# Performance work log

Hardware: AMD Instinct MI355X
Metric: run time of the kernel (lower is better)

Reference implementation:

```python
import jax, jax.numpy as jnp
import numpy as np

E = 2048      # embed_size
H = 16        # heads_size
D_HEAD = E // H          # 128
D_ROPE = 32
SPLIT = D_HEAD - D_ROPE  # 96
C = 512       # d_kv_comp
B, S = 2, 2048
ROT_SCALE = 40.0


def _rotary_emb(seq_len):
    # inv_freq has d_rope//4 entries; emb is [S, d_rope//2]
    half = D_ROPE // 2
    inv_freq = 1.0 / (10000.0 ** (jnp.arange(0, half, 2, dtype=jnp.float32) / half))
    t = jnp.arange(seq_len, dtype=jnp.float32) / ROT_SCALE
    freqs = jnp.einsum('i,j->ij', t, inv_freq)
    return jnp.concatenate([freqs, freqs], axis=-1)  # [S, d_rope//2]


def _rotate_half(x):
    x1, x2 = jnp.split(x, 2, axis=-1)
    return jnp.concatenate([-x2, x1], axis=-1)


def _apply_rotary(x, cos, sin):
    rd = cos.shape[-1]
    x_rot, x_base = x[..., :rd], x[..., rd:]
    x_rot = x_rot * cos + _rotate_half(x_rot) * sin
    return jnp.concatenate([x_rot, x_base], axis=-1)


def setup_inputs() -> dict:
    key = jax.random.key(0)
    ks = jax.random.split(key, 10)

    def xav(k, shape):
        fan_in, fan_out = shape
        lim = float(np.sqrt(6.0 / (fan_in + fan_out)))
        return jax.random.uniform(k, shape, jnp.float32, -lim, lim)

    return {
        'h': jax.random.normal(ks[0], (B, S, E), jnp.float32),
        'W_dkv': xav(ks[1], (E, C)), 'b_dkv': jnp.zeros((C,), jnp.float32),
        'W_dq':  xav(ks[2], (E, C)), 'b_dq':  jnp.zeros((C,), jnp.float32),
        'W_uk':  xav(ks[3], (C, H * SPLIT)),  'b_uk': jnp.zeros((H * SPLIT,), jnp.float32),
        'W_uv':  xav(ks[4], (C, H * D_HEAD)), 'b_uv': jnp.zeros((H * D_HEAD,), jnp.float32),
        'W_uq':  xav(ks[5], (C, H * SPLIT)),  'b_uq': jnp.zeros((H * SPLIT,), jnp.float32),
        'W_qr':  xav(ks[6], (C, H * D_ROPE)), 'b_qr': jnp.zeros((H * D_ROPE,), jnp.float32),
        'W_kr':  xav(ks[7], (E, H * D_ROPE)), 'b_kr': jnp.zeros((H * D_ROPE,), jnp.float32),
        'W_out': xav(ks[8], (H * D_HEAD, E)), 'b_out': jnp.zeros((E,), jnp.float32),
    }


def reference(h, W_dkv, b_dkv, W_dq, b_dq, W_uk, b_uk, W_uv, b_uv,
              W_uq, b_uq, W_qr, b_qr, W_kr, b_kr, W_out, b_out):
    Bq, Sq, _ = h.shape
    c_kv = h @ W_dkv + b_dkv                                   # [B,S,C]
    k = (c_kv @ W_uk + b_uk).reshape(Bq, Sq, H, SPLIT)
    v = (c_kv @ W_uv + b_uv).reshape(Bq, Sq, H, D_HEAD)
    c_q = h @ W_dq + b_dq
    q_base = (c_q @ W_uq + b_uq).reshape(Bq, Sq, H, SPLIT)
    q_rot = (c_q @ W_qr + b_qr).reshape(Bq, Sq, H, D_ROPE)

    emb = _rotary_emb(Sq)                                      # [S, d_rope//2]
    cos = jnp.cos(emb)[None, :, None, :]
    sin = jnp.sin(emb)[None, :, None, :]
    q_rot = _apply_rotary(q_rot, cos, sin)
    k_rot = _apply_rotary((h @ W_kr + b_kr).reshape(Bq, Sq, H, D_ROPE), cos, sin)

    q = jnp.concatenate([q_base, q_rot], axis=-1)              # [B,S,H,d_head]
    k_full = jnp.concatenate([k, k_rot], axis=-1)

    scores = jnp.einsum('bqhd,bkhd->bhqk', q, k_full) / jnp.sqrt(jnp.float32(D_HEAD))
    causal = jnp.tril(jnp.ones((Sq, Sq), dtype=bool))
    scores = jnp.where(causal[None, None], scores, -jnp.inf)
    attn = jax.nn.softmax(scores, axis=-1)
    out = jnp.einsum('bhqk,bkhd->bqhd', attn, v).reshape(Bq, Sq, H * D_HEAD)
    out = out @ W_out + b_out
    return out, c_kv, k_rot
```

## Files before the change

kernel.cpp:

```cpp
#include <hip/hip_runtime.h>
#include <hip/hip_bf16.h>

#define B_   2
#define S_   2048
#define E_   2048
#define H_   16
#define DH_  128
#define DR_  32
#define SP_  96
#define C_   512
#define M_   (B_ * S_)

#define LOG2E 1.4426950408889634f

typedef __attribute__((ext_vector_type(8))) short short8;
typedef __attribute__((ext_vector_type(4))) float floatx4;

__device__ __forceinline__ float bfu(unsigned short u) {
  return __uint_as_float((unsigned)u << 16);
}
__device__ __forceinline__ unsigned short f2bf(float f) {
  unsigned u = __float_as_uint(f);
  return (unsigned short)((u + 0x7fff + ((u >> 16) & 1)) >> 16);
}

__device__ __forceinline__ void gload16(const void* g, void* l) {
  __builtin_amdgcn_global_load_lds(
      (const __attribute__((address_space(1))) void*)g,
      (__attribute__((address_space(3))) void*)l, 16, 0, 0);
}

struct TEnt { const float* W; unsigned short* Wt; int K, N, ntiles, nx; };
struct TTab { TEnt e[8]; };

__global__ __launch_bounds__(256) void prep_kernel(
    const float* __restrict__ hsrc, unsigned short* __restrict__ hdst,
    TTab tab) {
  if (blockIdx.x < 8192) {
    size_t i = ((size_t)blockIdx.x * 256 + threadIdx.x) * 4;
    float4 v = *(const float4*)(hsrc + i);
    ushort4 w;
    w.x = f2bf(v.x); w.y = f2bf(v.y); w.z = f2bf(v.z); w.w = f2bf(v.w);
    *(ushort4*)(hdst + i) = w;
    return;
  }
  __shared__ unsigned short T[32][33];
  int rem = blockIdx.x - 8192;
  const float* W = nullptr; unsigned short* Wt = nullptr;
  int K = 0, N = 0, nx = 1;
  bool done = false;
#pragma unroll
  for (int j = 0; j < 8; j++) {
    if (!done) {
      if (rem < tab.e[j].ntiles) {
        W = tab.e[j].W; Wt = tab.e[j].Wt;
        K = tab.e[j].K; N = tab.e[j].N; nx = tab.e[j].nx;
        done = true;
      } else {
        rem -= tab.e[j].ntiles;
      }
    }
  }
  int n0 = (rem % nx) * 32, k0 = (rem / nx) * 32;
  int t = threadIdx.x, lane = t & 31, grp = t >> 5;
#pragma unroll
  for (int p = 0; p < 4; p++) {
    int k = p * 8 + grp;
    T[lane][k] = f2bf(W[(size_t)(k0 + k) * N + n0 + lane]);
  }
  __syncthreads();
#pragma unroll
  for (int p = 0; p < 4; p++) {
    int n = p * 8 + grp;
    Wt[(size_t)(n0 + n) * K + k0 + lane] = T[n][lane];
  }
}

struct Seg {
  float* outF;
  unsigned short* outB;
  const float* bias;
  const float* biasM;
  int orow, chunk, gstride, obase, nstart, ileave;
  float oscale;
};

__device__ __forceinline__ void gemm_body(
    const unsigned short* __restrict__ A, const unsigned short* __restrict__ W,
    int K, int bm, int bn, const Seg& sg) {
  __shared__ unsigned short As0[128 * 32];
  __shared__ unsigned short Bs0[128 * 32];
  __shared__ unsigned short As1[128 * 32];
  __shared__ unsigned short Bs1[128 * 32];
  int tid = threadIdx.x;
  int lane = tid & 63, wave = tid >> 6;
  int l16 = lane & 15, quad = lane >> 4;
  int wm = (wave & 1) * 64, wn = (wave >> 1) * 64;

  floatx4 acc[4][4];
#pragma unroll
  for (int mt = 0; mt < 4; mt++)
#pragma unroll
    for (int nt = 0; nt < 4; nt++) acc[mt][nt] = (floatx4){0.f, 0.f, 0.f, 0.f};

  int c0 = wave * 2, c1 = c0 + 1;
  int srow = lane >> 2, scol = (lane & 3) * 8;
  const unsigned short* Ag0 = A + (size_t)(bm + c0 * 16 + srow) * K + scol;
  const unsigned short* Ag1 = A + (size_t)(bm + c1 * 16 + srow) * K + scol;
  const unsigned short* Bg0 = W + (size_t)(bn + c0 * 16 + srow) * K + scol;
  const unsigned short* Bg1 = W + (size_t)(bn + c1 * 16 + srow) * K + scol;

#define GSTAGE(kk, Asb, Bsb) do {            \
    gload16(Ag0 + (kk), &Asb[c0 * 512]);     \
    gload16(Ag1 + (kk), &Asb[c1 * 512]);     \
    gload16(Bg0 + (kk), &Bsb[c0 * 512]);     \
    gload16(Bg1 + (kk), &Bsb[c1 * 512]); } while (0)

#define GCOMPUTE(Asb, Bsb) do {                                            \
    short8 af[4], bfv[4];                                                  \
    _Pragma("unroll")                                                      \
    for (int mt = 0; mt < 4; mt++)                                         \
      af[mt] = *(const short8*)&Asb[(wm + mt * 16 + l16) * 32 + quad * 8]; \
    _Pragma("unroll")                                                      \
    for (int nt = 0; nt < 4; nt++)                                         \
      bfv[nt] = *(const short8*)&Bsb[(wn + nt * 16 + l16) * 32 + quad * 8];\
    _Pragma("unroll")                                                      \
    for (int mt = 0; mt < 4; mt++)                                         \
      _Pragma("unroll")                                                    \
      for (int nt = 0; nt < 4; nt++)                                       \
        acc[mt][nt] = __builtin_amdgcn_mfma_f32_16x16x32_bf16(             \
            af[mt], bfv[nt], acc[mt][nt], 0, 0, 0); } while (0)

  GSTAGE(0, As0, Bs0);
  __syncthreads();
  for (int k0 = 0; k0 < K; k0 += 64) {
    GSTAGE(k0 + 32, As1, Bs1);
    GCOMPUTE(As0, Bs0);
    __syncthreads();
    if (k0 + 64 < K) GSTAGE(k0 + 64, As0, Bs0);
    GCOMPUTE(As1, Bs1);
    __syncthreads();
  }
#undef GSTAGE
#undef GCOMPUTE

#pragma unroll
  for (int mt = 0; mt < 4; mt++) {
    int m0 = bm + wm + mt * 16 + quad * 4;
    float bm4[4] = {0.f, 0.f, 0.f, 0.f};
    if (sg.biasM) {
#pragma unroll
      for (int r = 0; r < 4; r++) bm4[r] = sg.biasM[m0 + r];
    }
#pragma unroll
    for (int nt = 0; nt < 4; nt++) {
      int n = bn + wn + nt * 16 + l16;
      int nl = n - sg.nstart;
      float bv = sg.biasM ? 0.f : sg.bias[nl];
      int ncol = sg.obase + (nl / sg.chunk) * sg.gstride + (nl % sg.chunk);
      if (sg.ileave)
        ncol = (ncol & ~31) | ((ncol & 15) << 1) | ((ncol >> 4) & 1);
#pragma unroll
      for (int r = 0; r < 4; r++) {
        float val = (acc[mt][nt][r] + (sg.biasM ? bm4[r] : bv)) * sg.oscale;
        size_t idx = (size_t)(m0 + r) * sg.orow + ncol;
        if (sg.outF) sg.outF[idx] = val;
        if (sg.outB) sg.outB[idx] = f2bf(val);
      }
    }
  }
}

__global__ __launch_bounds__(256) void mfma_gemm(
    const unsigned short* __restrict__ A, const unsigned short* __restrict__ Wt,
    Seg s0, Seg s1, Seg s2, int K) {
  int gx = gridDim.x;
  int nwg = gx * gridDim.y;
  int flat = blockIdx.y * gx + blockIdx.x;
  int w = (flat & 7) * (nwg >> 3) + (flat >> 3);
  int by = w / gx, bx = w - by * gx;
  int bm = by * 128, bn = bx * 128;
  Seg sg = (bn >= s2.nstart) ? s2 : ((bn >= s1.nstart) ? s1 : s0);
  gemm_body(A, Wt, K, bm, bn, sg);
}

__global__ __launch_bounds__(256) void fused_gemm3(
    const unsigned short* __restrict__ ckv, const unsigned short* __restrict__ cq,
    const unsigned short* __restrict__ wuk, const unsigned short* __restrict__ wuv,
    const unsigned short* __restrict__ wuq,
    unsigned short* __restrict__ kbf, unsigned short* __restrict__ vtbf,
    unsigned short* __restrict__ qbf,
    const float* __restrict__ b_uk, const float* __restrict__ b_uv,
    const float* __restrict__ b_uq, const float* __restrict__ b_qr,
    float qscale) {
  int flat = blockIdx.x;
  int w = (flat & 7) * 176 + (flat >> 3);
  const unsigned short* A; const unsigned short* W;
  int bm, bn;
  Seg sg;
  sg.outF = nullptr; sg.oscale = 1.f; sg.ileave = 0; sg.nstart = 0;
  if (w < 384) {
    int by = w / 12, bx = w - by * 12;
    bm = by * 128; bn = bx * 128;
    A = ckv; W = wuk;
    sg.outB = kbf; sg.bias = b_uk; sg.biasM = nullptr;
    sg.orow = 2048; sg.chunk = SP_; sg.gstride = DH_; sg.obase = 0;
  } else if (w < 896) {
    int w2 = w - 384;
    int by = w2 >> 5, bx = w2 & 31;
    bm = by * 128; bn = bx * 128;
    A = wuv; W = ckv;
    sg.outB = vtbf; sg.bias = nullptr; sg.biasM = b_uv;
    sg.orow = M_; sg.chunk = M_; sg.gstride = M_; sg.obase = 0; sg.ileave = 1;
  } else {
    int w3 = w - 896;
    int by = w3 >> 4, bx = w3 & 15;
    bm = by * 128; bn = bx * 128;
    A = cq; W = wuq;
    sg.outB = qbf; sg.biasM = nullptr; sg.orow = 2048; sg.oscale = qscale;
    if (bn >= 1536) {
      sg.bias = b_qr; sg.chunk = DR_; sg.gstride = DH_; sg.obase = SP_;
      sg.nstart = 1536;
    } else {
      sg.bias = b_uq; sg.chunk = SP_; sg.gstride = DH_; sg.obase = 0;
    }
  }
  gemm_body(A, W, 512, bm, bn, sg);
}

__global__ __launch_bounds__(256) void rope_kernel(
    unsigned short* __restrict__ qf, unsigned short* __restrict__ kf,
    float* __restrict__ krot_out) {
  int idx = blockIdx.x * 256 + threadIdx.x;
  int j  = idx & 7;
  int h  = (idx >> 3) & (H_ - 1);
  int bs = idx >> 7;
  if (bs >= M_) return;
  int s = bs & (S_ - 1);
  float t = (float)s / 40.0f;
  float ang = t * exp2f(-1.6609640474436813f * (float)j);
  float c = cosf(ang), sn = sinf(ang);

  size_t base = (size_t)bs * 2048 + h * 128 + 96;
  float x0 = bfu(qf[base + j]), x1 = bfu(qf[base + j + 8]);
  qf[base + j]     = f2bf(x0 * c - x1 * sn);
  qf[base + j + 8] = f2bf(x1 * c + x0 * sn);

  float y0 = bfu(kf[base + j]), y1 = bfu(kf[base + j + 8]);
  float r0 = y0 * c - y1 * sn;
  float r1 = y1 * c + y0 * sn;
  kf[base + j]     = f2bf(r0);
  kf[base + j + 8] = f2bf(r1);

  size_t ko = (size_t)bs * (H_ * DR_) + h * DR_;
  krot_out[ko + j]      = r0;
  krot_out[ko + j + 8]  = r1;
  krot_out[ko + 16 + j] = bfu(kf[base + 16 + j]);
  krot_out[ko + 24 + j] = bfu(kf[base + 24 + j]);
}

#define PST 72
__global__ __launch_bounds__(256, 2) void attn_kernel(
    const unsigned short* __restrict__ qf, const unsigned short* __restrict__ kf,
    const unsigned short* __restrict__ vt, unsigned short* __restrict__ ao) {
  __shared__ unsigned short Ks[2][64 * 128];
  __shared__ unsigned short Vs[2][128 * 64];
  __shared__ unsigned short Ps[4][16 * PST];

  int bid0 = blockIdx.x;
  int xcd  = bid0 & 7;
  int idx  = bid0 >> 3;
  int r_   = idx >> 5;
  int q_   = idx & 31;
  int bh   = xcd * 4 + (q_ >> 3);
  int jp   = r_ ? (15 - (q_ & 7)) : (q_ & 7);
  int h    = bh & 15;
  int b    = bh >> 4;
  int jjh  = 31 - jp;
  int jjl  = jp;
  int q0h  = jjh << 6, q0l = jjl << 6;
  int nchunks = jjh + 1;

  int tid  = threadIdx.x;
  int wave = tid >> 6;
  int lane = tid & 63;
  int l16  = lane & 15;
  int quad = lane >> 4;
  int x7   = l16 & 7;

  int krow = tid >> 2;
  int kst  = (tid & 3) * 4;
  int vrow = tid >> 1;
  int vst  = (tid & 1) * 4;
  const unsigned short* kg =
      kf + ((size_t)(b * S_ + krow)) * 2048 + h * 128 + kst * 8;
  const unsigned short* vg =
      vt + ((size_t)(h * 128 + vrow)) * 4096 + b * 2048 + vst * 8;
  int kwl[4], vwl[4];
#pragma unroll
  for (int i = 0; i < 4; i++) {
    kwl[i] = krow * 128 + (((kst + i) ^ (krow & 7)) * 8);
    vwl[i] = vrow * 64  + (((vst + i) ^ (vrow & 7)) * 8);
  }

  short8 qfh[4], qfl[4];
  {
    const unsigned short* qb =
        qf + ((size_t)(b * S_ + q0h + wave * 16 + l16)) * 2048 + h * 128 + quad * 8;
#pragma unroll
    for (int c = 0; c < 4; c++) qfh[c] = *(const short8*)(qb + c * 32);
  }
  {
    const unsigned short* qb =
        qf + ((size_t)(b * S_ + q0l + wave * 16 + l16)) * 2048 + h * 128 + quad * 8;
#pragma unroll
    for (int c = 0; c < 4; c++) qfl[c] = *(const short8*)(qb + c * 32);
  }

  floatx4 OaccH[8], OaccL[8];
#pragma unroll
  for (int dt = 0; dt < 8; dt++) {
    OaccH[dt] = (floatx4){0.f, 0.f, 0.f, 0.f};
    OaccL[dt] = (floatx4){0.f, 0.f, 0.f, 0.f};
  }
  float lpH[4] = {0.f, 0.f, 0.f, 0.f};
  float lpL[4] = {0.f, 0.f, 0.f, 0.f};
  int qgh = q0h + wave * 16;
  int qgl = q0l + wave * 16;

#define SCOMPUTE(QF, OC, LP, QG, DIAG) do {                                   \
    const unsigned short* Kc = Ks[cur];                                       \
    const unsigned short* Vc = Vs[cur];                                       \
    floatx4 sv[4];                                                            \
    _Pragma("unroll")                                                         \
    for (int nt = 0; nt < 4; nt++) sv[nt] = (floatx4){0.f, 0.f, 0.f, 0.f};    \
    __builtin_amdgcn_s_setprio(1);                                            \
    _Pragma("unroll")                                                         \
    for (int nt = 0; nt < 4; nt++)                                            \
      _Pragma("unroll")                                                       \
      for (int c = 0; c < 4; c++) {                                           \
        short8 kfr = *(const short8*)&Kc[(nt * 16 + l16) * 128 +              \
                                         ((4 * c + quad) ^ x7) * 8];          \
        sv[nt] = __builtin_amdgcn_mfma_f32_16x16x32_bf16(QF[c], kfr, sv[nt],  \
                                                         0, 0, 0);            \
      }                                                                       \
    __builtin_amdgcn_s_setprio(0);                                            \
    unsigned short* P = Ps[wave];                                             \
    _Pragma("unroll")                                                         \
    for (int ks = 0; ks < 2; ks++)                                            \
      _Pragma("unroll")                                                       \
      for (int r = 0; r < 4; r++) {                                           \
        float p0 = exp2f(fminf(sv[2 * ks][r], 80.f));                         \
        float p1 = exp2f(fminf(sv[2 * ks + 1][r], 80.f));                     \
        if (DIAG) {                                                           \
          int q_r = QG + quad * 4 + r;                                        \
          int kc0 = kt0 + ks * 32 + l16;                                      \
          if (kc0 > q_r)      p0 = 0.f;                                       \
          if (kc0 + 16 > q_r) p1 = 0.f;                                       \
        }                                                                     \
        unsigned pk;                                                          \
        asm("v_cvt_pk_bf16_f32 %0, %1, %2" : "=v"(pk) : "v"(p0), "v"(p1));    \
        *(unsigned*)&P[(quad * 4 + r) * PST + ks * 32 + 2 * l16] = pk;        \
        LP[r] += p0 + p1;                                                     \
      }                                                                       \
    short8 pf0 = *(const short8*)&P[l16 * PST + quad * 8];                    \
    short8 pf1 = *(const short8*)&P[l16 * PST + 32 + quad * 8];               \
    __builtin_amdgcn_s_setprio(1);                                            \
    _Pragma("unroll")                                                         \
    for (int dt = 0; dt < 8; dt++) {                                          \
      short8 vf0 = *(const short8*)&Vc[(dt * 16 + l16) * 64 +                 \
                                       ((quad) ^ x7) * 8];                    \
      OC[dt] = __builtin_amdgcn_mfma_f32_16x16x32_bf16(pf0, vf0, OC[dt],      \
                                                       0, 0, 0);              \
      short8 vf1 = *(const short8*)&Vc[(dt * 16 + l16) * 64 +                 \
                                       ((4 + quad) ^ x7) * 8];                \
      OC[dt] = __builtin_amdgcn_mfma_f32_16x16x32_bf16(pf1, vf1, OC[dt],      \
                                                       0, 0, 0);              \
    }                                                                         \
    __builtin_amdgcn_s_setprio(0);                                            \
  } while (0)

  short8 kr[4], vr[4];
#pragma unroll
  for (int i = 0; i < 4; i++) {
    kr[i] = *(const short8*)(kg + i * 8);
    vr[i] = *(const short8*)(vg + i * 8);
  }
#pragma unroll
  for (int i = 0; i < 4; i++) {
    *(short8*)&Ks[0][kwl[i]] = kr[i];
    *(short8*)&Vs[0][vwl[i]] = vr[i];
  }
#pragma unroll
  for (int i = 0; i < 4; i++) {
    kr[i] = *(const short8*)(kg + 131072 + i * 8);
    vr[i] = *(const short8*)(vg + 64 + i * 8);
  }
  __syncthreads();

  int cur = 0;
  for (int t = 0; t < nchunks; t++) {
#pragma unroll
    for (int i = 0; i < 4; i++) {
      *(short8*)&Ks[cur ^ 1][kwl[i]] = kr[i];
      *(short8*)&Vs[cur ^ 1][vwl[i]] = vr[i];
    }
    {
      int tf = (t + 2 < nchunks) ? t + 2 : nchunks - 1;
      const unsigned short* ksrc = kg + (size_t)tf * 131072;
      const unsigned short* vsrc = vg + tf * 64;
#pragma unroll
      for (int i = 0; i < 4; i++) {
        kr[i] = *(const short8*)(ksrc + i * 8);
        vr[i] = *(const short8*)(vsrc + i * 8);
      }
    }
    int kt0 = t << 6;
    SCOMPUTE(qfh, OaccH, lpH, qgh, (t == jjh));
    if (t <= jjl) SCOMPUTE(qfl, OaccL, lpL, qgl, (t == jjl));
    __syncthreads();
    cur ^= 1;
  }
#undef SCOMPUTE

#pragma unroll
  for (int side = 0; side < 2; side++) {
    floatx4* OC = side ? OaccL : OaccH;
    float*   LP = side ? lpL : lpH;
    int qg = (side ? qgl : qgh) + quad * 4;
    float linv[4];
#pragma unroll
    for (int r = 0; r < 4; r++) {
      float ls = LP[r];
#pragma unroll
      for (int sh = 1; sh < 16; sh <<= 1) ls += __shfl_xor(ls, sh);
      linv[r] = 1.0f / ls;
    }
#pragma unroll
    for (int r = 0; r < 4; r++) {
      unsigned short* dst =
          ao + ((size_t)(b * S_ + qg + r)) * 2048 + h * 128 + l16;
#pragma unroll
      for (int dt = 0; dt < 8; dt++) dst[dt * 16] = f2bf(OC[dt][r] * linv[r]);
    }
  }
}

static inline Seg mkseg(float* oF, unsigned short* oB, const float* bias,
                        const float* biasM, int orow, int chunk, int gstride,
                        int obase, int nstart, int ileave, float oscale) {
  Seg s;
  s.outF = oF; s.outB = oB; s.bias = bias; s.biasM = biasM;
  s.orow = orow; s.chunk = chunk; s.gstride = gstride;
  s.obase = obase; s.nstart = nstart; s.ileave = ileave; s.oscale = oscale;
  return s;
}
static inline Seg segnone() {
  return mkseg(nullptr, nullptr, nullptr, nullptr, 1, 1, 1, 0, 0x7fffffff, 0, 1.f);
}
static inline TEnt mktent(const float* W, unsigned short* Wt, int K, int N,
                          int ntiles, int nx) {
  TEnt e;
  e.W = W; e.Wt = Wt; e.K = K; e.N = N; e.ntiles = ntiles; e.nx = nx;
  return e;
}

extern "C" void kernel_launch(void* const* d_in, const int* in_sizes, int n_in,
                              void* d_out, int out_size, void* d_ws, size_t ws_size,
                              hipStream_t stream) {
  const float* h     = (const float*)d_in[0];
  const float* W_dkv = (const float*)d_in[1];
  const float* b_dkv = (const float*)d_in[2];
  const float* W_dq  = (const float*)d_in[3];
  const float* b_dq  = (const float*)d_in[4];
  const float* W_uk  = (const float*)d_in[5];
  const float* b_uk  = (const float*)d_in[6];
  const float* W_uv  = (const float*)d_in[7];
  const float* b_uv  = (const float*)d_in[8];
  const float* W_uq  = (const float*)d_in[9];
  const float* b_uq  = (const float*)d_in[10];
  const float* W_qr  = (const float*)d_in[11];
  const float* b_qr  = (const float*)d_in[12];
  const float* W_kr  = (const float*)d_in[13];
  const float* b_kr  = (const float*)d_in[14];
  const float* W_out = (const float*)d_in[15];
  const float* b_out = (const float*)d_in[16];

  float* out      = (float*)d_out;
  float* out_ckv  = out + (size_t)M_ * E_;
  float* out_krot = out_ckv + (size_t)M_ * C_;

  unsigned short* w16 = (unsigned short*)d_ws;
  unsigned short* h_bf   = w16;
  unsigned short* q_bf   = w16 + 8388608;
  unsigned short* k_bf   = w16 + 16777216;
  unsigned short* vt_bf  = w16 + 25165824;
  unsigned short* ao_bf  = w16 + 33554432;
  unsigned short* ckv_bf = w16 + 41943040;
  unsigned short* cq_bf  = w16 + 44040192;
  unsigned short* Wt_dkv = w16 + 46137344;
  unsigned short* Wt_dq  = w16 + 47185920;
  unsigned short* Wt_kr  = w16 + 48234496;
  unsigned short* Wt_uk  = w16 + 49283072;
  unsigned short* Wt_uv  = w16 + 50069504;
  unsigned short* Wt_uq  = w16 + 51118080;
  unsigned short* Wt_qr  = w16 + 51904512;
  unsigned short* Wt_out = w16 + 52166656;
  (void)Wt_qr;

  dim3 blk(256);
  const float qscale = 0.08838834764831845f * LOG2E;

  TTab tab;
  tab.e[0] = mktent(W_dkv, Wt_dkv, E_, C_,       1024, 16);
  tab.e[1] = mktent(W_dq,  Wt_dq,  E_, C_,       1024, 16);
  tab.e[2] = mktent(W_kr,  Wt_kr,  E_, H_ * DR_, 1024, 16);
  tab.e[3] = mktent(W_uk,  Wt_uk,  C_, H_ * SP_,  768, 48);
  tab.e[4] = mktent(W_uv,  Wt_uv,  C_, H_ * DH_, 1024, 64);
  tab.e[5] = mktent(W_uq,  Wt_uq,  C_, H_ * SP_,  768, 48);
  tab.e[6] = mktent(W_qr,  w16 + 51904512, C_, H_ * DR_,  256, 16);
  tab.e[7] = mktent(W_out, Wt_out, E_, E_,       4096, 64);
  prep_kernel<<<18176, blk, 0, stream>>>(h, h_bf, tab);

  mfma_gemm<<<dim3(1536 / 128, M_ / 128), blk, 0, stream>>>(
      h_bf, Wt_dkv,
      mkseg(out_ckv, ckv_bf, b_dkv, nullptr, C_, C_, C_, 0, 0, 0, 1.f),
      mkseg(nullptr, cq_bf,  b_dq,  nullptr, C_, C_, C_, 0, 512, 0, 1.f),
      mkseg(nullptr, k_bf,   b_kr,  nullptr, 2048, DR_, DH_, SP_, 1024, 0, 1.f),
      E_);

  fused_gemm3<<<1408, blk, 0, stream>>>(
      ckv_bf, cq_bf, Wt_uk, Wt_uv, Wt_uq, k_bf, vt_bf, q_bf,
      b_uk, b_uv, b_uq, b_qr, qscale);

  rope_kernel<<<(M_ * H_ * 8) / 256, blk, 0, stream>>>(q_bf, k_bf, out_krot);
  attn_kernel<<<B_ * H_ * 16, blk, 0, stream>>>(q_bf, k_bf, vt_bf, ao_bf);

  mfma_gemm<<<dim3(E_ / 128, M_ / 128), blk, 0, stream>>>(
      ao_bf, Wt_out,
      mkseg(out, nullptr, b_out, nullptr, E_, E_, E_, 0, 0, 0, 1.f),
      segnone(), segnone(), E_);
}
```

Baseline: 353.7 us.

## Fuse RoPE into GEMM epilogues and widen GEMM blocks to 512 threads

Removes the standalone rope kernel and applies the rotary rotation inside the GEMM epilogues. The two rotated halves are exchanged with a lane shuffle, and the fp32 k_rot output is written straight from the first projection GEMM. Separately, the GEMM workgroups grow from 4 to 8 waves, each computing a 32x64 subtile with half the accumulators, which lowers register pressure per wave. This trades an extra launch and a bf16 round-trip for trig work in the epilogue, and changes per-wave MFMA density and occupancy.

```diff
diff --git a/kernel.cpp b/kernel.cpp
--- a/kernel.cpp
+++ b/kernel.cpp
@@ -81,7 +81,8 @@
   unsigned short* outB;
   const float* bias;
   const float* biasM;
-  int orow, chunk, gstride, obase, nstart, ileave;
+  float* krotF;
+  int orow, chunk, gstride, obase, nstart, ileave, rope;
   float oscale;
 };
 
@@ -95,37 +96,33 @@
   int tid = threadIdx.x;
   int lane = tid & 63, wave = tid >> 6;
   int l16 = lane & 15, quad = lane >> 4;
-  int wm = (wave & 1) * 64, wn = (wave >> 1) * 64;
-
-  floatx4 acc[4][4];
-#pragma unroll
-  for (int mt = 0; mt < 4; mt++)
+  int wm = (wave & 3) * 32, wn = (wave >> 2) * 64;
+
+  floatx4 acc[2][4];
+#pragma unroll
+  for (int mt = 0; mt < 2; mt++)
 #pragma unroll
     for (int nt = 0; nt < 4; nt++) acc[mt][nt] = (floatx4){0.f, 0.f, 0.f, 0.f};
 
-  int c0 = wave * 2, c1 = c0 + 1;
   int srow = lane >> 2, scol = (lane & 3) * 8;
-  const unsigned short* Ag0 = A + (size_t)(bm + c0 * 16 + srow) * K + scol;
-  const unsigned short* Ag1 = A + (size_t)(bm + c1 * 16 + srow) * K + scol;
-  const unsigned short* Bg0 = W + (size_t)(bn + c0 * 16 + srow) * K + scol;
-  const unsigned short* Bg1 = W + (size_t)(bn + c1 * 16 + srow) * K + scol;
-
-#define GSTAGE(kk, Asb, Bsb) do {            \
-    gload16(Ag0 + (kk), &Asb[c0 * 512]);     \
-    gload16(Ag1 + (kk), &Asb[c1 * 512]);     \
-    gload16(Bg0 + (kk), &Bsb[c0 * 512]);     \
-    gload16(Bg1 + (kk), &Bsb[c1 * 512]); } while (0)
+  const unsigned short* Ag = A + (size_t)(bm + wave * 16 + srow) * K + scol;
+  const unsigned short* Bg = W + (size_t)(bn + wave * 16 + srow) * K + scol;
+  int lo = wave * 512;
+
+#define GSTAGE(kk, Asb, Bsb) do {      \
+    gload16(Ag + (kk), &Asb[lo]);      \
+    gload16(Bg + (kk), &Bsb[lo]); } while (0)
 
 #define GCOMPUTE(Asb, Bsb) do {                                            \
-    short8 af[4], bfv[4];                                                  \
+    short8 af[2], bfv[4];                                                  \
     _Pragma("unroll")                                                      \
-    for (int mt = 0; mt < 4; mt++)                                         \
+    for (int mt = 0; mt < 2; mt++)                                         \
       af[mt] = *(const short8*)&Asb[(wm + mt * 16 + l16) * 32 + quad * 8]; \
     _Pragma("unroll")                                                      \
     for (int nt = 0; nt < 4; nt++)                                         \
       bfv[nt] = *(const short8*)&Bsb[(wn + nt * 16 + l16) * 32 + quad * 8];\
     _Pragma("unroll")                                                      \
-    for (int mt = 0; mt < 4; mt++)                                         \
+    for (int mt = 0; mt < 2; mt++)                                         \
       _Pragma("unroll")                                                    \
       for (int nt = 0; nt < 4; nt++)                                       \
         acc[mt][nt] = __builtin_amdgcn_mfma_f32_16x16x32_bf16(             \
@@ -145,7 +142,7 @@
 #undef GCOMPUTE
 
 #pragma unroll
-  for (int mt = 0; mt < 4; mt++) {
+  for (int mt = 0; mt < 2; mt++) {
     int m0 = bm + wm + mt * 16 + quad * 4;
     float bm4[4] = {0.f, 0.f, 0.f, 0.f};
     if (sg.biasM) {
@@ -160,9 +157,21 @@
       int ncol = sg.obase + (nl / sg.chunk) * sg.gstride + (nl % sg.chunk);
       if (sg.ileave)
         ncol = (ncol & ~31) | ((ncol & 15) << 1) | ((ncol >> 4) & 1);
+      bool rot_half = sg.rope && ((nl & 31) < 16);
 #pragma unroll
       for (int r = 0; r < 4; r++) {
         float val = (acc[mt][nt][r] + (sg.biasM ? bm4[r] : bv)) * sg.oscale;
+        if (rot_half) {
+          int j = l16 & 7;
+          int srw = (m0 + r) & (S_ - 1);
+          float ang = ((float)srw / 40.0f) *
+                      exp2f(-1.6609640474436813f * (float)j);
+          float cc = cosf(ang), ss = sinf(ang);
+          float part = __shfl_xor(val, 8);
+          val = (l16 < 8) ? (val * cc - part * ss) : (val * cc + part * ss);
+        }
+        if (sg.rope == 1 && sg.krotF)
+          sg.krotF[(size_t)(m0 + r) * (H_ * DR_) + nl] = val;
         size_t idx = (size_t)(m0 + r) * sg.orow + ncol;
         if (sg.outF) sg.outF[idx] = val;
         if (sg.outB) sg.outB[idx] = f2bf(val);
@@ -171,7 +180,7 @@
   }
 }
 
-__global__ __launch_bounds__(256) void mfma_gemm(
+__global__ __launch_bounds__(512) void mfma_gemm(
     const unsigned short* __restrict__ A, const unsigned short* __restrict__ Wt,
     Seg s0, Seg s1, Seg s2, int K) {
   int gx = gridDim.x;
@@ -184,7 +193,7 @@
   gemm_body(A, Wt, K, bm, bn, sg);
 }
 
-__global__ __launch_bounds__(256) void fused_gemm3(
+__global__ __launch_bounds__(512) void fused_gemm3(
     const unsigned short* __restrict__ ckv, const unsigned short* __restrict__ cq,
     const unsigned short* __restrict__ wuk, const unsigned short* __restrict__ wuv,
     const unsigned short* __restrict__ wuq,
@@ -199,6 +208,7 @@
   int bm, bn;
   Seg sg;
   sg.outF = nullptr; sg.oscale = 1.f; sg.ileave = 0; sg.nstart = 0;
+  sg.rope = 0; sg.krotF = nullptr;
   if (w < 384) {
     int by = w / 12, bx = w - by * 12;
     bm = by * 128; bn = bx * 128;
@@ -220,43 +230,12 @@
     sg.outB = qbf; sg.biasM = nullptr; sg.orow = 2048; sg.oscale = qscale;
     if (bn >= 1536) {
       sg.bias = b_qr; sg.chunk = DR_; sg.gstride = DH_; sg.obase = SP_;
-      sg.nstart = 1536;
+      sg.nstart = 1536; sg.rope = 2;
     } else {
       sg.bias = b_uq; sg.chunk = SP_; sg.gstride = DH_; sg.obase = 0;
     }
   }
   gemm_body(A, W, 512, bm, bn, sg);
-}
-
-__global__ __launch_bounds__(256) void rope_kernel(
-    unsigned short* __restrict__ qf, unsigned short* __restrict__ kf,
-    float* __restrict__ krot_out) {
-  int idx = blockIdx.x * 256 + threadIdx.x;
-  int j  = idx & 7;
-  int h  = (idx >> 3) & (H_ - 1);
-  int bs = idx >> 7;
-  if (bs >= M_) return;
-  int s = bs & (S_ - 1);
-  float t = (float)s / 40.0f;
-  float ang = t * exp2f(-1.6609640474436813f * (float)j);
-  float c = cosf(ang), sn = sinf(ang);
-
-  size_t base = (size_t)bs * 2048 + h * 128 + 96;
-  float x0 = bfu(qf[base + j]), x1 = bfu(qf[base + j + 8]);
-  qf[base + j]     = f2bf(x0 * c - x1 * sn);
-  qf[base + j + 8] = f2bf(x1 * c + x0 * sn);
-
-  float y0 = bfu(kf[base + j]), y1 = bfu(kf[base + j + 8]);
-  float r0 = y0 * c - y1 * sn;
-  float r1 = y1 * c + y0 * sn;
-  kf[base + j]     = f2bf(r0);
-  kf[base + j + 8] = f2bf(r1);
-
-  size_t ko = (size_t)bs * (H_ * DR_) + h * DR_;
-  krot_out[ko + j]      = r0;
-  krot_out[ko + j + 8]  = r1;
-  krot_out[ko + 16 + j] = bfu(kf[base + 16 + j]);
-  krot_out[ko + 24 + j] = bfu(kf[base + 24 + j]);
 }
 
 #define PST 72
@@ -448,15 +427,18 @@
 
 static inline Seg mkseg(float* oF, unsigned short* oB, const float* bias,
                         const float* biasM, int orow, int chunk, int gstride,
-                        int obase, int nstart, int ileave, float oscale) {
+                        int obase, int nstart, int ileave, float oscale,
+                        int rope, float* krotF) {
   Seg s;
-  s.outF = oF; s.outB = oB; s.bias = bias; s.biasM = biasM;
+  s.outF = oF; s.outB = oB; s.bias = bias; s.biasM = biasM; s.krotF = krotF;
   s.orow = orow; s.chunk = chunk; s.gstride = gstride;
-  s.obase = obase; s.nstart = nstart; s.ileave = ileave; s.oscale = oscale;
+  s.obase = obase; s.nstart = nstart; s.ileave = ileave; s.rope = rope;
+  s.oscale = oscale;
   return s;
 }
 static inline Seg segnone() {
-  return mkseg(nullptr, nullptr, nullptr, nullptr, 1, 1, 1, 0, 0x7fffffff, 0, 1.f);
+  return mkseg(nullptr, nullptr, nullptr, nullptr, 1, 1, 1, 0, 0x7fffffff,
+               0, 1.f, 0, nullptr);
 }
 static inline TEnt mktent(const float* W, unsigned short* Wt, int K, int N,
                           int ntiles, int nx) {
@@ -508,7 +490,7 @@
   unsigned short* Wt_out = w16 + 52166656;
   (void)Wt_qr;
 
-  dim3 blk(256);
+  dim3 blk256(256), blk512(512);
   const float qscale = 0.08838834764831845f * LOG2E;
 
   TTab tab;
@@ -520,24 +502,24 @@
   tab.e[5] = mktent(W_uq,  Wt_uq,  C_, H_ * SP_,  768, 48);
   tab.e[6] = mktent(W_qr,  w16 + 51904512, C_, H_ * DR_,  256, 16);
   tab.e[7] = mktent(W_out, Wt_out, E_, E_,       4096, 64);
-  prep_kernel<<<18176, blk, 0, stream>>>(h, h_bf, tab);
-
-  mfma_gemm<<<dim3(1536 / 128, M_ / 128), blk, 0, stream>>>(
+  prep_kernel<<<18176, blk256, 0, stream>>>(h, h_bf, tab);
+
+  mfma_gemm<<<dim3(1536 / 128, M_ / 128), blk512, 0, stream>>>(
       h_bf, Wt_dkv,
-      mkseg(out_ckv, ckv_bf, b_dkv, nullptr, C_, C_, C_, 0, 0, 0, 1.f),
-      mkseg(nullptr, cq_bf,  b_dq,  nullptr, C_, C_, C_, 0, 512, 0, 1.f),
-      mkseg(nullptr, k_bf,   b_kr,  nullptr, 2048, DR_, DH_, SP_, 1024, 0, 1.f),
+      mkseg(out_ckv, ckv_bf, b_dkv, nullptr, C_, C_, C_, 0, 0, 0, 1.f, 0, nullptr),
+      mkseg(nullptr, cq_bf,  b_dq,  nullptr, C_, C_, C_, 0, 512, 0, 1.f, 0, nullptr),
+      mkseg(nullptr, k_bf,   b_kr,  nullptr, 2048, DR_, DH_, SP_, 1024, 0, 1.f,
+            1, out_krot),
       E_);
 
-  fused_gemm3<<<1408, blk, 0, stream>>>(
+  fused_gemm3<<<1408, blk512, 0, stream>>>(
       ckv_bf, cq_bf, Wt_uk, Wt_uv, Wt_uq, k_bf, vt_bf, q_bf,
       b_uk, b_uv, b_uq, b_qr, qscale);
 
-  rope_kernel<<<(M_ * H_ * 8) / 256, blk, 0, stream>>>(q_bf, k_bf, out_krot);
-  attn_kernel<<<B_ * H_ * 16, blk, 0, stream>>>(q_bf, k_bf, vt_bf, ao_bf);
-
-  mfma_gemm<<<dim3(E_ / 128, M_ / 128), blk, 0, stream>>>(
+  attn_kernel<<<B_ * H_ * 16, blk256, 0, stream>>>(q_bf, k_bf, vt_bf, ao_bf);
+
+  mfma_gemm<<<dim3(E_ / 128, M_ / 128), blk512, 0, stream>>>(
       ao_bf, Wt_out,
-      mkseg(out, nullptr, b_out, nullptr, E_, E_, E_, 0, 0, 0, 1.f),
+      mkseg(out, nullptr, b_out, nullptr, E_, E_, E_, 0, 0, 0, 1.f, 0, nullptr),
       segnone(), segnone(), E_);
 }
```

Measured after the change: 362.9 us. +2.6%, slower.
